# Performance work log

Hardware: AMD Instinct MI355X
Metric: run time of the kernel (lower is better)

Reference implementation:

```python
import jax, jax.numpy as jnp
import numpy as np

T, B, E, H, V = 128, 64, 300, 2048, 50000


def setup_inputs() -> dict:
    key = jax.random.key(0)
    ks = jax.random.split(key, 7)
    tokens = jax.random.randint(ks[0], (T, B), 0, V, dtype=jnp.int32)
    lens = jax.random.randint(ks[1], (B,), 1, T + 1, dtype=jnp.int32)  # lens >= 1 (assert 0 not in lens)
    embed_table = jax.random.normal(ks[2], (V, E), dtype=jnp.float32) * 0.1
    W_ih = jax.random.normal(ks[3], (4 * H, E), dtype=jnp.float32) * 0.02
    W_hh = jax.random.normal(ks[4], (4 * H, H), dtype=jnp.float32) * 0.02
    b_ih = jax.random.normal(ks[5], (4 * H,), dtype=jnp.float32) * 0.02
    b_hh = jax.random.normal(ks[6], (4 * H,), dtype=jnp.float32) * 0.02
    return {"tokens": tokens, "lens": lens, "embed_table": embed_table,
            "W_ih": W_ih, "W_hh": W_hh, "b_ih": b_ih, "b_hh": b_hh}


def _lstm_scan(xs, W_ih, W_hh, bias, reverse):
    # xs: [T, B, E]; returns all hidden states [T, B, H] (in scan order) and final (h, c)
    hdim = W_hh.shape[1]
    bsz = xs.shape[1]
    h0 = jnp.zeros((bsz, hdim), xs.dtype)
    c0 = jnp.zeros((bsz, hdim), xs.dtype)

    def step(carry, x):
        h, c = carry
        gates = x @ W_ih.T + h @ W_hh.T + bias  # [B, 4H]
        i, f, g, o = jnp.split(gates, 4, axis=-1)  # PyTorch LSTMCell gate order: i, f, g, o
        i = jax.nn.sigmoid(i)
        f = jax.nn.sigmoid(f)
        g = jnp.tanh(g)
        o = jax.nn.sigmoid(o)
        c = f * c + i * g
        h = o * jnp.tanh(c)
        return (h, c), h

    (h_fin, c_fin), hs = jax.lax.scan(step, (h0, c0), xs, reverse=reverse)
    return hs, h_fin


def reference(tokens, lens, embed_table, W_ih, W_hh, b_ih, b_hh):
    # tokens: [T, B] int ids (time-major, matching input_[i] loop over dim 0)
    x = embed_table[tokens]  # [T, B, E]
    bias = b_ih + b_hh
    hs_fwd, _ = _lstm_scan(x, W_ih, W_hh, bias, reverse=False)   # [T, B, H]
    _, h_bwd = _lstm_scan(x, W_ih, W_hh, bias, reverse=True)     # [B, H], same shared cell
    bsz = tokens.shape[1]
    # forward hidden at the last valid timestep of each example (lens - 1)
    last_fwd = hs_fwd[lens - 1, jnp.arange(bsz)]  # [B, H]
    return jnp.concatenate([last_fwd, h_bwd], axis=1)  # [B, 2H]
```

## Files before the change

### kernel.cpp

```cpp
#include <hip/hip_runtime.h>
#include <math.h>

#define T_ 128
#define B_ 64
#define E_ 300
#define H_ 2048

#define K1   2368
#define XKS  10
#define NKS  74
#define APELEMS 19398656ull
#define BXELEMS 5242880ull
#define BHPING  524288ull

typedef __attribute__((ext_vector_type(8))) short short8;
typedef __attribute__((ext_vector_type(4))) float float4v;

__device__ __forceinline__ unsigned f2bf(float f) {
    unsigned u = __float_as_uint(f);
    return (u + 0x7FFFu + ((u >> 16) & 1u)) >> 16;
}
__device__ __forceinline__ float bf2f(unsigned b) { return __uint_as_float(b << 16); }

__device__ __forceinline__ void gl_lds16(const void* g, void* l) {
    __builtin_amdgcn_global_load_lds(
        (const __attribute__((address_space(1))) unsigned int*)g,
        (__attribute__((address_space(3))) unsigned int*)l, 16, 0, 0);
}

__device__ __forceinline__ float sigm(float x) { return 1.f / (1.f + expf(-x)); }


__global__ void init2(short* __restrict__ Bh, float* __restrict__ cb) {
    const int nB = 2 * (int)BHPING;
    const int nC = 2 * 2048 * 64;
    int stride = gridDim.x * blockDim.x;
    int i = blockIdx.x * blockDim.x + threadIdx.x;
    for (int idx = i; idx < nB; idx += stride) Bh[idx] = 0;
    for (int idx = i; idx < nC; idx += stride) cb[idx] = 0.f;
}

__global__ void pack_w(const float* __restrict__ Wih, const float* __restrict__ Whh,
                       short* __restrict__ Ahi, short* __restrict__ Alo) {
    long long idx = (long long)blockIdx.x * blockDim.x + threadIdx.x;
    if (idx >= (long long)APELEMS) return;
    int j  = (int)(idx & 7);
    int l  = (int)((idx >> 3) & 63);
    int mf = (int)((idx >> 9) & 7);
    int rest = (int)(idx >> 12);
    int ks = rest % 74;
    int rb = rest / 74;
    int row = rb * 128 + mf * 16 + (l & 15);
    int kr  = ks * 32 + (l >> 4) * 8 + j;
    float wv = 0.f;
    if (kr < 300)       wv = Wih[(size_t)row * 300 + kr];
    else if (kr >= 320) wv = Whh[(size_t)row * 2048 + (kr - 320)];
    unsigned hb = f2bf(wv);
    Ahi[idx] = (short)hb;
    Alo[idx] = (short)f2bf(wv - bf2f(hb));
}

__global__ void pack_x(const int* __restrict__ tokens, const float* __restrict__ embed,
                       short* __restrict__ Bx) {
    long long idx = (long long)blockIdx.x * blockDim.x + threadIdx.x;
    if (idx >= (long long)BXELEMS) return;
    int j   = (int)(idx & 7);
    int l   = (int)((idx >> 3) & 63);
    int nf4 = (int)((idx >> 9) & 3);
    int hl  = (int)((idx >> 11) & 1);
    int rest = (int)(idx >> 12);
    int ks = rest % 10;
    int tt = rest / 10;
    int b  = nf4 * 16 + (l & 15);
    int kr = ks * 32 + (l >> 4) * 8 + j;
    float v = 0.f;
    if (kr < 300) {
        int tok = tokens[tt * 64 + b];
        v = embed[(size_t)tok * 300 + kr];
    }
    unsigned hb = f2bf(v);
    Bx[idx] = hl ? (short)f2bf(v - bf2f(hb)) : (short)hb;
}

template<int HI>
__device__ __forceinline__ void pass10(
    const short* __restrict__ ApB,
    const short* __restrict__ Bx,
    const short* __restrict__ BhP,
    short* lds, float4v (&acc)[4][4],
    int ks0, int nks, int t, int tid, int wm, int wn, int l, int boff)
{
    auto stage = [&](int ks, int buf) {
        short* As = lds + buf * 12288;
        short* Bs = As + 4096;
        const short* aB = ApB + (size_t)ks * 4096;
        gl_lds16(aB + tid * 8, As + tid * 8);
        gl_lds16(aB + 2048 + tid * 8, As + 2048 + tid * 8);
        constexpr int NBL = HI ? 4 : 2;
#pragma unroll
        for (int q = 0; q < NBL; ++q) {
            constexpr_int:;
            const int dsel = HI ? (q >> 1) : q;
            const int hl   = HI ? (q & 1) : 0;
            const short* base;
            if (ks < XKS) {
                const int xt = dsel ? (127 - t) : t;
                base = Bx + (size_t)(((xt * 10 + ks) * 2 + hl) * 4) * 512;
            } else {
                base = BhP + (size_t)((ks - 10) * 16 + (dsel * 2 + hl) * 4) * 512;
            }
            gl_lds16(base + boff, Bs + q * 2048 + tid * 8);
        }
    };

    stage(ks0, 0);
    stage(ks0 + 1, 1);
    if constexpr (HI) { asm volatile("s_waitcnt vmcnt(6)" ::: "memory"); }
    else              { asm volatile("s_waitcnt vmcnt(4)" ::: "memory"); }
    __builtin_amdgcn_s_barrier();
    __builtin_amdgcn_sched_barrier(0);

    for (int it = 0; it < nks; ++it) {
        const int buf = it % 3;
        stage(ks0 + it + 2, (it + 2) % 3);

        short* As = lds + buf * 12288;
        short* Bs = As + 4096;
        short8 a[4];
#pragma unroll
        for (int i = 0; i < 4; ++i)
            a[i] = *(const short8*)(As + ((wm * 4 + i) * 64 + l) * 8);

        if constexpr (HI) {
            short8 bf[8];
#pragma unroll
            for (int j = 0; j < 8; ++j)
                bf[j] = *(const short8*)(Bs + ((wn * 8 + j) * 64 + l) * 8);
            __builtin_amdgcn_s_setprio(1);
#pragma unroll
            for (int i = 0; i < 4; ++i)
#pragma unroll
                for (int h2 = 0; h2 < 2; ++h2)
#pragma unroll
                    for (int n = 0; n < 4; ++n)
                        acc[i][n] = __builtin_amdgcn_mfma_f32_16x16x32_bf16(
                            a[i], bf[h2 * 4 + n], acc[i][n], 0, 0, 0);
            __builtin_amdgcn_s_setprio(0);
        } else {
            short8 bf[4];
#pragma unroll
            for (int n = 0; n < 4; ++n)
                bf[n] = *(const short8*)(Bs + ((wn * 4 + n) * 64 + l) * 8);
            __builtin_amdgcn_s_setprio(1);
#pragma unroll
            for (int i = 0; i < 4; ++i)
#pragma unroll
                for (int n = 0; n < 4; ++n)
                    acc[i][n] = __builtin_amdgcn_mfma_f32_16x16x32_bf16(
                        a[i], bf[n], acc[i][n], 0, 0, 0);
            __builtin_amdgcn_s_setprio(0);
        }

        if constexpr (HI) { asm volatile("s_waitcnt vmcnt(6)" ::: "memory"); }
        else              { asm volatile("s_waitcnt vmcnt(4)" ::: "memory"); }
        __builtin_amdgcn_s_barrier();
        __builtin_amdgcn_sched_barrier(0);
    }

    asm volatile("s_waitcnt vmcnt(0)" ::: "memory");
    __builtin_amdgcn_s_barrier();
    __builtin_amdgcn_sched_barrier(0);
}

__global__ __launch_bounds__(256, 2) void gemm_step(
    const short* __restrict__ Ahi, const short* __restrict__ Alo,
    const short* __restrict__ Bx, const short* __restrict__ Bh,
    float* __restrict__ p, int t)
{
    __shared__ short lds[36864];
    const int bb = (int)blockIdx.x;
    const int mb = bb >> 3, s = bb & 7;
    const int tid = (int)threadIdx.x;
    const int w = tid >> 6, l = tid & 63;
    const int wm = w >> 1, wn = w & 1;
    const int ping = t & 1;
    const int ks0 = (s < 2) ? s * 10 : 20 + (s - 2) * 9;
    const int nks = (s < 2) ? 10 : 9;
    const int boff = w * 512 + l * 8;
    const short* BhP = Bh + (size_t)ping * BHPING;

    float4v acc[4][4];
#pragma unroll
    for (int i = 0; i < 4; ++i)
#pragma unroll
        for (int n = 0; n < 4; ++n) acc[i][n] = (float4v){0.f, 0.f, 0.f, 0.f};

    pass10<1>(Ahi + (size_t)mb * 74 * 4096, Bx, BhP, lds, acc,
              ks0, nks, t, tid, wm, wn, l, boff);
    pass10<0>(Alo + (size_t)mb * 74 * 4096, Bx, BhP, lds, acc,
              ks0, nks, t, tid, wm, wn, l, boff);

#pragma unroll
    for (int i = 0; i < 4; ++i)
#pragma unroll
        for (int n = 0; n < 4; ++n)
#pragma unroll
            for (int r = 0; r < 4; ++r) {
                int row = mb * 128 + wm * 64 + i * 16 + (l >> 4) * 4 + r;
                int col = wn * 64 + n * 16 + (l & 15);
                p[((size_t)s * 8192 + row) * 128 + col] = acc[i][n][r];
            }
}

__global__ __launch_bounds__(256) void update2(
    const float* __restrict__ p,
    const float* __restrict__ b_ih, const float* __restrict__ b_hh,
    const int* __restrict__ lens,
    float* __restrict__ cbuf,
    short* __restrict__ Bh,
    float* __restrict__ out, int t)
{
    int tid0 = blockIdx.x * 256 + threadIdx.x;
    for (int item = tid0; item < 262144; item += 65536) {
        int b = item & 63, k = (item >> 6) & 2047, dir = item >> 17;
        float g[4];
#pragma unroll
        for (int gg = 0; gg < 4; ++gg) {
            int row = gg * 2048 + k;
            float v = 0.f;
#pragma unroll
            for (int s = 0; s < 8; ++s) v += p[((size_t)s * 8192 + row) * 128 + dir * 64 + b];
            g[gg] = v + b_ih[row] + b_hh[row];
        }
        float iv = sigm(g[0]);
        float fv = sigm(g[1]);
        float gv = tanhf(g[2]);
        float ov = sigm(g[3]);
        size_t cidx = ((size_t)dir * 2048 + k) * 64 + b;
        float c = fv * cbuf[cidx] + iv * gv;
        cbuf[cidx] = c;
        float h = ov * tanhf(c);

        int kk = k & 31, ksh = k >> 5;
        int jj = kk & 7, ll = (kk >> 3) * 16 + (b & 15), sub = b >> 4;
        int pingW = (t + 1) & 1;
        size_t baseh = (size_t)pingW * BHPING + ((size_t)ksh * 16 + (dir * 2) * 4 + sub) * 512 + ll * 8 + jj;
        size_t basel = (size_t)pingW * BHPING + ((size_t)ksh * 16 + (dir * 2 + 1) * 4 + sub) * 512 + ll * 8 + jj;
        unsigned hb = f2bf(h);
        Bh[baseh] = (short)hb;
        Bh[basel] = (short)f2bf(h - bf2f(hb));

        if (dir == 0) { if (t == lens[b] - 1) out[(size_t)b * 4096 + k] = h; }
        else          { if (t == 127)         out[(size_t)b * 4096 + 2048 + k] = h; }
    }
}

#define R2K1    2368
#define R2EPAD  304
#define R2HOFF  304
#define R2HEND  2352
#define R2SEGSTEPS 74
#define R2REALSTEPS 222
#define R2SPLITSTEPS 56

__global__ void init_ws2(short* __restrict__ hb, float* __restrict__ cb,
                         short* __restrict__ zer) {
    const int nH = 2 * 2 * 2 * 64 * 2048;
    const int nC = 2 * 2048 * 64;
    int stride = gridDim.x * blockDim.x;
    int i = blockIdx.x * blockDim.x + threadIdx.x;
    for (int idx = i; idx < nH; idx += stride) hb[idx] = 0;
    for (int idx = i; idx < nC; idx += stride) cb[idx] = 0.f;
    for (int idx = i; idx < 128; idx += stride) zer[idx] = 0;
}

__global__ void conv_w(const float* __restrict__ Wih, const float* __restrict__ Whh,
                       short* __restrict__ whi, short* __restrict__ wlo) {
    int idx = blockIdx.x * blockDim.x + threadIdx.x;
    const int total = 8192 * R2K1;
    if (idx >= total) return;
    int j = idx / R2K1;
    int col = idx - j * R2K1;
    float w = 0.f;
    if (col < E_) w = Wih[(size_t)j * E_ + col];
    else if (col >= R2HOFF && col < R2HEND) w = Whh[(size_t)j * H_ + (col - R2HOFF)];
    unsigned hb = f2bf(w);
    whi[idx] = (short)hb;
    wlo[idx] = (short)f2bf(w - bf2f(hb));
}

__global__ void conv_x(const int* __restrict__ tokens, const float* __restrict__ embed,
                       short* __restrict__ xhi, short* __restrict__ xlo) {
    int idx = blockIdx.x * blockDim.x + threadIdx.x;
    const int total = T_ * B_ * R2EPAD;
    if (idx >= total) return;
    int t = idx / (B_ * R2EPAD);
    int r = idx - t * (B_ * R2EPAD);
    int bb = r / R2EPAD;
    int e = r - bb * R2EPAD;
    float v = 0.f;
    if (e < E_) {
        int tok = tokens[t * B_ + bb];
        v = embed[(size_t)tok * E_ + e];
    }
    unsigned hb = f2bf(v);
    xhi[idx] = (short)hb;
    xlo[idx] = (short)f2bf(v - bf2f(hb));
}

__global__ __launch_bounds__(512) void gemm_partial(
    const short* __restrict__ Whi, const short* __restrict__ Wlo,
    const short* __restrict__ xhi, const short* __restrict__ xlo,
    const short* __restrict__ hbuf,
    const short* __restrict__ zeros,
    float* __restrict__ pbuf, int t)
{
    __shared__ short As[2][8192];
    __shared__ short Bs[2][2048];

    const int bx  = blockIdx.x;
    const int s   = bx & 3;
    const int kt  = (bx >> 2) & 31;
    const int dir = bx >> 7;
    const int tid = threadIdx.x;
    const int w   = tid >> 6;
    const int l   = tid & 63;
    const int ping = t & 1;
    const int xt   = dir ? (T_ - 1 - t) : t;

    int jA[2], cA[2];
#pragma unroll
    for (int q = 0; q < 2; ++q) {
        int idx = (w * 2 + q) * 64 + l;
        cA[q] = idx >> 8;
        int row = idx & 255;
        jA[q] = (row >> 6) * 2048 + kt * 64 + (row & 63);
    }
    int cB = 0, bB = 0;
    if (w < 4) { int idx = w * 64 + l; cB = idx >> 6; bB = idx & 63; }

    const int lhi = l >> 4, llo = l & 15;
    const int rowbase = (w >> 1) * 64 + (w & 1) * 32;

    float4v acc[2][4];
#pragma unroll
    for (int a = 0; a < 2; ++a)
#pragma unroll
        for (int b = 0; b < 4; ++b) acc[a][b] = (float4v){0.f, 0.f, 0.f, 0.f};

    auto stage = [&](int g, int buf) {
        const bool dummy = (g >= R2REALSTEPS);
        const int seg = dummy ? 2 : g / R2SEGSTEPS;
        const int ss  = dummy ? 0 : g - seg * R2SEGSTEPS;
        const int kbase = ss * 32;
        const short* Wsel = (seg < 2) ? Whi : Wlo;
        const int hl = (seg == 1) ? 1 : 0;
        const short* xsel = (seg == 1) ? xlo : xhi;
        const short* hsel = hbuf + (((size_t)ping * 2 + hl) * 2 + dir) * (64 * 2048);
#pragma unroll
        for (int q = 0; q < 2; ++q) {
            const short* src = Wsel + (size_t)jA[q] * R2K1 + kbase + 8 * cA[q];
            gl_lds16(src, &As[buf][(w * 2 + q) * 64 * 8]);
        }
        if (w < 4) {
            int row8 = kbase + 8 * cB;
            const short* src;
            if (dummy || row8 >= R2HEND) src = zeros;
            else if (row8 < R2EPAD)      src = xsel + ((size_t)xt * 64 + bB) * R2EPAD + row8;
            else                         src = hsel + (size_t)bB * 2048 + (row8 - R2HOFF);
            gl_lds16(src, &Bs[buf][w * 64 * 8]);
        }
    };

    const int g0 = s * R2SPLITSTEPS;
    stage(g0, 0);

    for (int it = 0; it < R2SPLITSTEPS; ++it) {
        const int buf = it & 1;
        if (it + 1 < R2SPLITSTEPS) stage(g0 + it + 1, buf ^ 1);
        __syncthreads();
        short8 a0 = *(const short8*)&As[buf][(lhi * 256 + rowbase + llo) * 8];
        short8 a1 = *(const short8*)&As[buf][(lhi * 256 + rowbase + 16 + llo) * 8];
        short8 b0 = *(const short8*)&Bs[buf][(lhi * 64 + llo) * 8];
        short8 b1 = *(const short8*)&Bs[buf][(lhi * 64 + 16 + llo) * 8];
        short8 b2 = *(const short8*)&Bs[buf][(lhi * 64 + 32 + llo) * 8];
        short8 b3 = *(const short8*)&Bs[buf][(lhi * 64 + 48 + llo) * 8];
        acc[0][0] = __builtin_amdgcn_mfma_f32_16x16x32_bf16(a0, b0, acc[0][0], 0, 0, 0);
        acc[0][1] = __builtin_amdgcn_mfma_f32_16x16x32_bf16(a0, b1, acc[0][1], 0, 0, 0);
        acc[0][2] = __builtin_amdgcn_mfma_f32_16x16x32_bf16(a0, b2, acc[0][2], 0, 0, 0);
        acc[0][3] = __builtin_amdgcn_mfma_f32_16x16x32_bf16(a0, b3, acc[0][3], 0, 0, 0);
        acc[1][0] = __builtin_amdgcn_mfma_f32_16x16x32_bf16(a1, b0, acc[1][0], 0, 0, 0);
        acc[1][1] = __builtin_amdgcn_mfma_f32_16x16x32_bf16(a1, b1, acc[1][1], 0, 0, 0);
        acc[1][2] = __builtin_amdgcn_mfma_f32_16x16x32_bf16(a1, b2, acc[1][2], 0, 0, 0);
        acc[1][3] = __builtin_amdgcn_mfma_f32_16x16x32_bf16(a1, b3, acc[1][3], 0, 0, 0);
        __syncthreads();
    }

    float* pb = pbuf + (((size_t)(dir * 32 + kt) * 4 + s) * 256) * 64;
#pragma unroll
    for (int qm = 0; qm < 2; ++qm)
#pragma unroll
        for (int nb = 0; nb < 4; ++nb)
#pragma unroll
            for (int r = 0; r < 4; ++r) {
                int row = rowbase + qm * 16 + lhi * 4 + r;
                int col = nb * 16 + llo;
                pb[row * 64 + col] = acc[qm][nb][r];
            }
}

__global__ __launch_bounds__(256) void lstm_update(
    const float* __restrict__ pbuf,
    const float* __restrict__ b_ih, const float* __restrict__ b_hh,
    const int* __restrict__ lens,
    float* __restrict__ cbuf,
    short* __restrict__ hbuf,
    float* __restrict__ out, int t)
{
    const int bx = blockIdx.x;
    const int kt = bx & 31, dir = bx >> 5;
    const float* pb = pbuf + (size_t)(dir * 32 + kt) * 4 * 256 * 64;
    const int ping = (t + 1) & 1;

    for (int idx = threadIdx.x; idx < 4096; idx += 256) {
        const int q = idx >> 6, bb = idx & 63;
        const int k = kt * 64 + q;
        float gv[4];
#pragma unroll
        for (int gg = 0; gg < 4; ++gg) {
            const int r = gg * 64 + q;
            float v = 0.f;
#pragma unroll
            for (int s2 = 0; s2 < 4; ++s2) v += pb[(s2 * 256 + r) * 64 + bb];
            const int j = gg * 2048 + k;
            gv[gg] = v + b_ih[j] + b_hh[j];
        }
        const float iv = sigm(gv[0]);
        const float fv = sigm(gv[1]);
        const float g2 = tanhf(gv[2]);
        const float ov = sigm(gv[3]);
        const size_t cidx = ((size_t)dir * 2048 + k) * 64 + bb;
        const float c = fv * cbuf[cidx] + iv * g2;
        cbuf[cidx] = c;
        const float h = ov * tanhf(c);

        const unsigned hb = f2bf(h);
        const float hhi = bf2f(hb);
        const unsigned lb = f2bf(h - hhi);
        const size_t basehi = (((size_t)ping * 2 + 0) * 2 + dir) * (64 * 2048);
        const size_t baselo = (((size_t)ping * 2 + 1) * 2 + dir) * (64 * 2048);
        hbuf[basehi + (size_t)bb * 2048 + k] = (short)hb;
        hbuf[baselo + (size_t)bb * 2048 + k] = (short)lb;

        if (dir == 0) {
            if (t == lens[bb] - 1) out[(size_t)bb * (2 * H_) + k] = h;
        } else {
            if (t == T_ - 1) out[(size_t)bb * (2 * H_) + H_ + k] = h;
        }
    }
}

__global__ void init_state(float* __restrict__ hbuf, float* __restrict__ cbuf) {
    int n_h = 2 * 2 * H_ * B_;
    int n_c = 2 * H_ * B_;
    int stride = gridDim.x * blockDim.x;
    int i = blockIdx.x * blockDim.x + threadIdx.x;
    for (int idx = i; idx < n_h; idx += stride) hbuf[idx] = 0.f;
    for (int idx = i; idx < n_c; idx += stride) cbuf[idx] = 0.f;
}

__global__ void gather_x(const int* __restrict__ tokens, const float* __restrict__ embed,
                         float* __restrict__ x_t) {
    int idx = blockIdx.x * blockDim.x + threadIdx.x;
    int total = T_ * E_ * B_;
    if (idx >= total) return;
    int b = idx % B_;
    int r = idx / B_;
    int e = r % E_;
    int t = r / E_;
    int tok = tokens[t * B_ + b];
    x_t[idx] = embed[tok * E_ + e];
}

__global__ __launch_bounds__(256) void lstm_step(
    const float* __restrict__ x_t, const float* __restrict__ W_ih,
    const float* __restrict__ W_hh, const float* __restrict__ b_ih,
    const float* __restrict__ b_hh, const int* __restrict__ lens,
    const float* __restrict__ h_in, float* __restrict__ h_out,
    float* __restrict__ cbuf, float* __restrict__ out, int t)
{
    const int dir = blockIdx.x >> 8;
    const int kblk = blockIdx.x & 255;
    const int bpair = threadIdx.x & 31;
    const int kloc = threadIdx.x >> 5;
    const int k = kblk * 8 + kloc;
    const int b0 = bpair * 2;
    const int xt = dir ? (T_ - 1 - t) : t;
    const float* xrow = x_t + (size_t)xt * E_ * B_;
    const float* hrow = h_in + (size_t)dir * H_ * B_;
    float a0x = 0.f, a0y = 0.f, a1x = 0.f, a1y = 0.f;
    float a2x = 0.f, a2y = 0.f, a3x = 0.f, a3y = 0.f;
    {
        const float* w0 = W_ih + (size_t)(0 * H_ + k) * E_;
        const float* w1 = W_ih + (size_t)(1 * H_ + k) * E_;
        const float* w2 = W_ih + (size_t)(2 * H_ + k) * E_;
        const float* w3 = W_ih + (size_t)(3 * H_ + k) * E_;
#pragma unroll 4
        for (int kk = 0; kk < E_; ++kk) {
            float2 xv = *(const float2*)(xrow + kk * B_ + b0);
            float c0 = w0[kk], c1 = w1[kk], c2 = w2[kk], c3 = w3[kk];
            a0x += xv.x * c0; a0y += xv.y * c0;
            a1x += xv.x * c1; a1y += xv.y * c1;
            a2x += xv.x * c2; a2y += xv.y * c2;
            a3x += xv.x * c3; a3y += xv.y * c3;
        }
    }
    {
        const float* w0 = W_hh + (size_t)(0 * H_ + k) * H_;
        const float* w1 = W_hh + (size_t)(1 * H_ + k) * H_;
        const float* w2 = W_hh + (size_t)(2 * H_ + k) * H_;
        const float* w3 = W_hh + (size_t)(3 * H_ + k) * H_;
#pragma unroll 4
        for (int kk = 0; kk < H_; ++kk) {
            float2 hv = *(const float2*)(hrow + kk * B_ + b0);
            float c0 = w0[kk], c1 = w1[kk], c2 = w2[kk], c3 = w3[kk];
            a0x += hv.x * c0; a0y += hv.y * c0;
            a1x += hv.x * c1; a1y += hv.y * c1;
            a2x += hv.x * c2; a2y += hv.y * c2;
            a3x += hv.x * c3; a3y += hv.y * c3;
        }
    }
    const int j0 = 0 * H_ + k, j1 = 1 * H_ + k, j2 = 2 * H_ + k, j3 = 3 * H_ + k;
    const float bi = b_ih[j0] + b_hh[j0];
    const float bf = b_ih[j1] + b_hh[j1];
    const float bg = b_ih[j2] + b_hh[j2];
    const float bo = b_ih[j3] + b_hh[j3];
    float* cdir = cbuf + (size_t)dir * H_ * B_;
    float* hdir = h_out + (size_t)dir * H_ * B_;
#pragma unroll
    for (int s = 0; s < 2; ++s) {
        const int b = b0 + s;
        const float ai = (s == 0) ? a0x : a0y;
        const float af = (s == 0) ? a1x : a1y;
        const float ag = (s == 0) ? a2x : a2y;
        const float ao = (s == 0) ? a3x : a3y;
        const float iv = sigm(ai + bi);
        const float fv = sigm(af + bf);
        const float gv = tanhf(ag + bg);
        const float ov = sigm(ao + bo);
        const int sidx = k * B_ + b;
        const float c_old = cdir[sidx];
        const float c_new = fv * c_old + iv * gv;
        cdir[sidx] = c_new;
        const float h_new = ov * tanhf(c_new);
        hdir[sidx] = h_new;
        if (dir == 0) {
            if (t == lens[b] - 1) out[(size_t)b * (2 * H_) + k] = h_new;
        } else {
            if (t == T_ - 1) out[(size_t)b * (2 * H_) + H_ + k] = h_new;
        }
    }
}

extern "C" void kernel_launch(void* const* d_in, const int* in_sizes, int n_in,
                              void* d_out, int out_size, void* d_ws, size_t ws_size,
                              hipStream_t stream) {
    const int*   tokens = (const int*)d_in[0];
    const int*   lens   = (const int*)d_in[1];
    const float* embed  = (const float*)d_in[2];
    const float* W_ih   = (const float*)d_in[3];
    const float* W_hh   = (const float*)d_in[4];
    const float* b_ih   = (const float*)d_in[5];
    const float* b_hh   = (const float*)d_in[6];
    float* out = (float*)d_out;

    short* Ahi = (short*)d_ws;
    short* Alo = Ahi + APELEMS;
    short* BxP = Alo + APELEMS;
    short* BhP = BxP + BXELEMS;
    float* cb2n = (float*)(BhP + 2 * BHPING);
    float* pP   = cb2n + 262144;
    const size_t req_new = (size_t)((char*)(pP + 8388608) - (char*)d_ws);

    const size_t SZ_W  = (size_t)8192 * R2K1;
    const size_t SZ_X  = (size_t)T_ * B_ * R2EPAD;
    const size_t SZ_HB = (size_t)2 * 2 * 2 * 64 * 2048;
    const size_t SZ_CB = (size_t)2 * 2048 * 64;
    const size_t SZ_PB = (size_t)64 * 4 * 256 * 64;
    short* Whi2  = (short*)d_ws;
    short* Wlo2  = Whi2 + SZ_W;
    short* xhiB = Wlo2 + SZ_W;
    short* xloB = xhiB + SZ_X;
    short* hb2  = xloB + SZ_X;
    short* zer  = hb2 + SZ_HB;
    float* cb2  = (float*)(zer + 128);
    float* pbuf = cb2 + SZ_CB;
    const size_t req_r2 = (size_t)((char*)(pbuf + SZ_PB) - (char*)d_ws);

    if (ws_size >= req_new) {
        init2<<<512, 256, 0, stream>>>(BhP, cb2n);
        pack_w<<<(int)((APELEMS + 255) / 256), 256, 0, stream>>>(W_ih, W_hh, Ahi, Alo);
        pack_x<<<(int)((BXELEMS + 255) / 256), 256, 0, stream>>>(tokens, embed, BxP);
        for (int t = 0; t < T_; ++t) {
            gemm_step<<<512, 256, 0, stream>>>(Ahi, Alo, BxP, BhP, pP, t);
            update2<<<256, 256, 0, stream>>>(pP, b_ih, b_hh, lens, cb2n, BhP, out, t);
        }
    } else if (ws_size >= req_r2) {
        init_ws2<<<1024, 256, 0, stream>>>(hb2, cb2, zer);
        {
            int total = 8192 * R2K1;
            conv_w<<<(total + 255) / 256, 256, 0, stream>>>(W_ih, W_hh, Whi2, Wlo2);
        }
        {
            int total = T_ * B_ * R2EPAD;
            conv_x<<<(total + 255) / 256, 256, 0, stream>>>(tokens, embed, xhiB, xloB);
        }
        for (int t = 0; t < T_; ++t) {
            gemm_partial<<<256, 512, 0, stream>>>(Whi2, Wlo2, xhiB, xloB, hb2, zer, pbuf, t);
            lstm_update<<<64, 256, 0, stream>>>(pbuf, b_ih, b_hh, lens, cb2, hb2, out, t);
        }
    } else {
        float* ws   = (float*)d_ws;
        float* x_t  = ws;
        float* hbuf = x_t + (size_t)T_ * E_ * B_;
        float* cbuf = hbuf + (size_t)2 * 2 * H_ * B_;
        init_state<<<256, 256, 0, stream>>>(hbuf, cbuf);
        {
            int total = T_ * E_ * B_;
            gather_x<<<(total + 255) / 256, 256, 0, stream>>>(tokens, embed, x_t);
        }
        for (int t = 0; t < T_; ++t) {
            const float* h_in  = hbuf + (size_t)(t & 1) * 2 * H_ * B_;
            float*       h_out = hbuf + (size_t)((t + 1) & 1) * 2 * H_ * B_;
            lstm_step<<<512, 256, 0, stream>>>(x_t, W_ih, W_hh, b_ih, b_hh, lens,
                                               h_in, h_out, cbuf, out, t);
        }
    }
}
```

Baseline: 4.005 ms.

## Vectorize LSTM update h writes per k-octet and stagger hi/lo GEMM passes

The update kernel now has each thread handle 8 consecutive hidden units for one batch element. It writes the bf16 hi/lo h values as single 16-byte short8 stores instead of scattered 2-byte stores, and reads lens once. The grid shrinks to 256 blocks of 128 threads, which lowers thread-level parallelism. Separately, the GEMM step alternates the order of its Ahi and Alo passes across blocks so neighbouring blocks do not stream the same weight half at the same moment.

```diff
diff --git a/kernel.cpp b/kernel.cpp
--- a/kernel.cpp
+++ b/kernel.cpp
@@ -99,7 +99,6 @@
         constexpr int NBL = HI ? 4 : 2;
 #pragma unroll
         for (int q = 0; q < NBL; ++q) {
-            constexpr_int:;
             const int dsel = HI ? (q >> 1) : q;
             const int hl   = HI ? (q & 1) : 0;
             const short* base;
@@ -195,10 +194,18 @@
 #pragma unroll
         for (int n = 0; n < 4; ++n) acc[i][n] = (float4v){0.f, 0.f, 0.f, 0.f};
 
-    pass10<1>(Ahi + (size_t)mb * 74 * 4096, Bx, BhP, lds, acc,
-              ks0, nks, t, tid, wm, wn, l, boff);
-    pass10<0>(Alo + (size_t)mb * 74 * 4096, Bx, BhP, lds, acc,
-              ks0, nks, t, tid, wm, wn, l, boff);
+    const int stag = (bb & 1) ^ ((bb >> 8) & 1);
+    if (stag == 0) {
+        pass10<1>(Ahi + (size_t)mb * 74 * 4096, Bx, BhP, lds, acc,
+                  ks0, nks, t, tid, wm, wn, l, boff);
+        pass10<0>(Alo + (size_t)mb * 74 * 4096, Bx, BhP, lds, acc,
+                  ks0, nks, t, tid, wm, wn, l, boff);
+    } else {
+        pass10<0>(Alo + (size_t)mb * 74 * 4096, Bx, BhP, lds, acc,
+                  ks0, nks, t, tid, wm, wn, l, boff);
+        pass10<1>(Ahi + (size_t)mb * 74 * 4096, Bx, BhP, lds, acc,
+                  ks0, nks, t, tid, wm, wn, l, boff);
+    }
 
 #pragma unroll
     for (int i = 0; i < 4; ++i)
@@ -212,7 +219,7 @@
             }
 }
 
-__global__ __launch_bounds__(256) void update2(
+__global__ __launch_bounds__(128) void update3(
     const float* __restrict__ p,
     const float* __restrict__ b_ih, const float* __restrict__ b_hh,
     const int* __restrict__ lens,
@@ -220,38 +227,75 @@
     short* __restrict__ Bh,
     float* __restrict__ out, int t)
 {
-    int tid0 = blockIdx.x * 256 + threadIdx.x;
-    for (int item = tid0; item < 262144; item += 65536) {
-        int b = item & 63, k = (item >> 6) & 2047, dir = item >> 17;
-        float g[4];
+    const int tid = (int)(blockIdx.x * 128 + threadIdx.x);
+    const int b    = tid & 63;
+    const int kOct = (tid >> 6) & 255;
+    const int dir  = tid >> 14;
+    const int k0   = kOct * 8;
+
+    float g[4][8];
+#pragma unroll
+    for (int gg = 0; gg < 4; ++gg)
+#pragma unroll
+        for (int j = 0; j < 8; ++j) g[gg][j] = 0.f;
+
+    for (int s = 0; s < 8; ++s) {
 #pragma unroll
         for (int gg = 0; gg < 4; ++gg) {
-            int row = gg * 2048 + k;
-            float v = 0.f;
-#pragma unroll
-            for (int s = 0; s < 8; ++s) v += p[((size_t)s * 8192 + row) * 128 + dir * 64 + b];
-            g[gg] = v + b_ih[row] + b_hh[row];
-        }
-        float iv = sigm(g[0]);
-        float fv = sigm(g[1]);
-        float gv = tanhf(g[2]);
-        float ov = sigm(g[3]);
-        size_t cidx = ((size_t)dir * 2048 + k) * 64 + b;
-        float c = fv * cbuf[cidx] + iv * gv;
+            const float* pr = p + ((size_t)s * 8192 + gg * 2048 + k0) * 128 + dir * 64 + b;
+#pragma unroll
+            for (int j = 0; j < 8; ++j)
+                g[gg][j] += pr[(size_t)j * 128];
+        }
+    }
+#pragma unroll
+    for (int gg = 0; gg < 4; ++gg)
+#pragma unroll
+        for (int j = 0; j < 8; ++j) {
+            int row = gg * 2048 + k0 + j;
+            g[gg][j] += b_ih[row] + b_hh[row];
+        }
+
+    const int ksh = k0 >> 5;
+    const int kk8 = (k0 & 31) >> 3;
+    const int ll  = kk8 * 16 + (b & 15);
+    const int sub = b >> 4;
+    const int pingW = (t + 1) & 1;
+    const int len_b = lens[b];
+
+    short8 vh, vl;
+    float outv[8];
+#pragma unroll
+    for (int j = 0; j < 8; ++j) {
+        const int k = k0 + j;
+        const float iv = sigm(g[0][j]);
+        const float fv = sigm(g[1][j]);
+        const float gv = tanhf(g[2][j]);
+        const float ov = sigm(g[3][j]);
+        const size_t cidx = ((size_t)dir * 2048 + k) * 64 + b;
+        const float c = fv * cbuf[cidx] + iv * gv;
         cbuf[cidx] = c;
-        float h = ov * tanhf(c);
-
-        int kk = k & 31, ksh = k >> 5;
-        int jj = kk & 7, ll = (kk >> 3) * 16 + (b & 15), sub = b >> 4;
-        int pingW = (t + 1) & 1;
-        size_t baseh = (size_t)pingW * BHPING + ((size_t)ksh * 16 + (dir * 2) * 4 + sub) * 512 + ll * 8 + jj;
-        size_t basel = (size_t)pingW * BHPING + ((size_t)ksh * 16 + (dir * 2 + 1) * 4 + sub) * 512 + ll * 8 + jj;
-        unsigned hb = f2bf(h);
-        Bh[baseh] = (short)hb;
-        Bh[basel] = (short)f2bf(h - bf2f(hb));
-
-        if (dir == 0) { if (t == lens[b] - 1) out[(size_t)b * 4096 + k] = h; }
-        else          { if (t == 127)         out[(size_t)b * 4096 + 2048 + k] = h; }
+        const float h = ov * tanhf(c);
+        const unsigned hb = f2bf(h);
+        vh[j] = (short)hb;
+        vl[j] = (short)f2bf(h - bf2f(hb));
+        outv[j] = h;
+    }
+    const size_t baseh = (size_t)pingW * BHPING + ((size_t)ksh * 16 + (dir * 2) * 4 + sub) * 512 + ll * 8;
+    const size_t basel = (size_t)pingW * BHPING + ((size_t)ksh * 16 + (dir * 2 + 1) * 4 + sub) * 512 + ll * 8;
+    *(short8*)(Bh + baseh) = vh;
+    *(short8*)(Bh + basel) = vl;
+
+    if (dir == 0) {
+        if (t == len_b - 1) {
+#pragma unroll
+            for (int j = 0; j < 8; ++j) out[(size_t)b * 4096 + k0 + j] = outv[j];
+        }
+    } else {
+        if (t == 127) {
+#pragma unroll
+            for (int j = 0; j < 8; ++j) out[(size_t)b * 4096 + 2048 + k0 + j] = outv[j];
+        }
     }
 }
 
@@ -603,7 +647,7 @@
         pack_x<<<(int)((BXELEMS + 255) / 256), 256, 0, stream>>>(tokens, embed, BxP);
         for (int t = 0; t < T_; ++t) {
             gemm_step<<<512, 256, 0, stream>>>(Ahi, Alo, BxP, BhP, pP, t);
-            update2<<<256, 256, 0, stream>>>(pP, b_ih, b_hh, lens, cb2n, BhP, out, t);
+            update3<<<256, 128, 0, stream>>>(pP, b_ih, b_hh, lens, cb2n, BhP, out, t);
         }
     } else if (ws_size >= req_r2) {
         init_ws2<<<1024, 256, 0, stream>>>(hb2, cb2, zer);
```

Result: slower. 4.241 ms (+5.9%).

## Fuse hi and lo weight passes into one double-buffered K loop

Applied to the files above, without the earlier changes.

The two separate passes over the K range (hi-part weights, then lo-part weights), each reloading the B tiles, are merged into one loop. Each stage now loads both the Ahi and Alo tiles plus all B tiles, so B is fetched from global memory once per k-slice instead of twice. Pipelining drops from triple to double buffering with a barrier before compute, which reduces prefetch depth and may expose more load latency.

```diff
diff --git a/kernel.cpp b/kernel.cpp
--- a/kernel.cpp
+++ b/kernel.cpp
@@ -82,102 +82,12 @@
     Bx[idx] = hl ? (short)f2bf(v - bf2f(hb)) : (short)hb;
 }
 
-template<int HI>
-__device__ __forceinline__ void pass10(
-    const short* __restrict__ ApB,
-    const short* __restrict__ Bx,
-    const short* __restrict__ BhP,
-    short* lds, float4v (&acc)[4][4],
-    int ks0, int nks, int t, int tid, int wm, int wn, int l, int boff)
-{
-    auto stage = [&](int ks, int buf) {
-        short* As = lds + buf * 12288;
-        short* Bs = As + 4096;
-        const short* aB = ApB + (size_t)ks * 4096;
-        gl_lds16(aB + tid * 8, As + tid * 8);
-        gl_lds16(aB + 2048 + tid * 8, As + 2048 + tid * 8);
-        constexpr int NBL = HI ? 4 : 2;
-#pragma unroll
-        for (int q = 0; q < NBL; ++q) {
-            constexpr_int:;
-            const int dsel = HI ? (q >> 1) : q;
-            const int hl   = HI ? (q & 1) : 0;
-            const short* base;
-            if (ks < XKS) {
-                const int xt = dsel ? (127 - t) : t;
-                base = Bx + (size_t)(((xt * 10 + ks) * 2 + hl) * 4) * 512;
-            } else {
-                base = BhP + (size_t)((ks - 10) * 16 + (dsel * 2 + hl) * 4) * 512;
-            }
-            gl_lds16(base + boff, Bs + q * 2048 + tid * 8);
-        }
-    };
-
-    stage(ks0, 0);
-    stage(ks0 + 1, 1);
-    if constexpr (HI) { asm volatile("s_waitcnt vmcnt(6)" ::: "memory"); }
-    else              { asm volatile("s_waitcnt vmcnt(4)" ::: "memory"); }
-    __builtin_amdgcn_s_barrier();
-    __builtin_amdgcn_sched_barrier(0);
-
-    for (int it = 0; it < nks; ++it) {
-        const int buf = it % 3;
-        stage(ks0 + it + 2, (it + 2) % 3);
-
-        short* As = lds + buf * 12288;
-        short* Bs = As + 4096;
-        short8 a[4];
-#pragma unroll
-        for (int i = 0; i < 4; ++i)
-            a[i] = *(const short8*)(As + ((wm * 4 + i) * 64 + l) * 8);
-
-        if constexpr (HI) {
-            short8 bf[8];
-#pragma unroll
-            for (int j = 0; j < 8; ++j)
-                bf[j] = *(const short8*)(Bs + ((wn * 8 + j) * 64 + l) * 8);
-            __builtin_amdgcn_s_setprio(1);
-#pragma unroll
-            for (int i = 0; i < 4; ++i)
-#pragma unroll
-                for (int h2 = 0; h2 < 2; ++h2)
-#pragma unroll
-                    for (int n = 0; n < 4; ++n)
-                        acc[i][n] = __builtin_amdgcn_mfma_f32_16x16x32_bf16(
-                            a[i], bf[h2 * 4 + n], acc[i][n], 0, 0, 0);
-            __builtin_amdgcn_s_setprio(0);
-        } else {
-            short8 bf[4];
-#pragma unroll
-            for (int n = 0; n < 4; ++n)
-                bf[n] = *(const short8*)(Bs + ((wn * 4 + n) * 64 + l) * 8);
-            __builtin_amdgcn_s_setprio(1);
-#pragma unroll
-            for (int i = 0; i < 4; ++i)
-#pragma unroll
-                for (int n = 0; n < 4; ++n)
-                    acc[i][n] = __builtin_amdgcn_mfma_f32_16x16x32_bf16(
-                        a[i], bf[n], acc[i][n], 0, 0, 0);
-            __builtin_amdgcn_s_setprio(0);
-        }
-
-        if constexpr (HI) { asm volatile("s_waitcnt vmcnt(6)" ::: "memory"); }
-        else              { asm volatile("s_waitcnt vmcnt(4)" ::: "memory"); }
-        __builtin_amdgcn_s_barrier();
-        __builtin_amdgcn_sched_barrier(0);
-    }
-
-    asm volatile("s_waitcnt vmcnt(0)" ::: "memory");
-    __builtin_amdgcn_s_barrier();
-    __builtin_amdgcn_sched_barrier(0);
-}
-
 __global__ __launch_bounds__(256, 2) void gemm_step(
     const short* __restrict__ Ahi, const short* __restrict__ Alo,
     const short* __restrict__ Bx, const short* __restrict__ Bh,
     float* __restrict__ p, int t)
 {
-    __shared__ short lds[36864];
+    __shared__ short lds[32768];
     const int bb = (int)blockIdx.x;
     const int mb = bb >> 3, s = bb & 7;
     const int tid = (int)threadIdx.x;
@@ -186,8 +96,9 @@
     const int ping = t & 1;
     const int ks0 = (s < 2) ? s * 10 : 20 + (s - 2) * 9;
     const int nks = (s < 2) ? 10 : 9;
-    const int boff = w * 512 + l * 8;
-    const short* BhP = Bh + (size_t)ping * BHPING;
+    const short* AhiB = Ahi + (size_t)mb * 74 * 4096;
+    const short* AloB = Alo + (size_t)mb * 74 * 4096;
+    const short* BhP  = Bh + (size_t)ping * BHPING;
 
     float4v acc[4][4];
 #pragma unroll
@@ -195,10 +106,73 @@
 #pragma unroll
         for (int n = 0; n < 4; ++n) acc[i][n] = (float4v){0.f, 0.f, 0.f, 0.f};
 
-    pass10<1>(Ahi + (size_t)mb * 74 * 4096, Bx, BhP, lds, acc,
-              ks0, nks, t, tid, wm, wn, l, boff);
-    pass10<0>(Alo + (size_t)mb * 74 * 4096, Bx, BhP, lds, acc,
-              ks0, nks, t, tid, wm, wn, l, boff);
+    auto stage = [&](int ks, int buf) {
+        short* As = lds + buf * 16384;
+        short* Al = As + 4096;
+        short* Bs = As + 8192;
+        const short* aH = AhiB + (size_t)ks * 4096;
+        const short* aL = AloB + (size_t)ks * 4096;
+        gl_lds16(aH + tid * 8,        As + tid * 8);
+        gl_lds16(aH + 2048 + tid * 8, As + 2048 + tid * 8);
+        gl_lds16(aL + tid * 8,        Al + tid * 8);
+        gl_lds16(aL + 2048 + tid * 8, Al + 2048 + tid * 8);
+#pragma unroll
+        for (int q = 0; q < 4; ++q) {
+            const int dsel = q >> 1, hl = q & 1;
+            const short* base;
+            if (ks < XKS) {
+                const int xt = dsel ? (127 - t) : t;
+                base = Bx + (size_t)(((xt * 10 + ks) * 2 + hl) * 4) * 512;
+            } else {
+                base = BhP + (size_t)((ks - 10) * 16 + (dsel * 2 + hl) * 4) * 512;
+            }
+            gl_lds16(base + tid * 8, Bs + q * 2048 + tid * 8);
+        }
+    };
+
+    stage(ks0, 0);
+    for (int it = 0; it < nks; ++it) {
+        stage(ks0 + it + 1, (it + 1) & 1);
+        asm volatile("s_waitcnt vmcnt(8)" ::: "memory");
+        __builtin_amdgcn_s_barrier();
+        __builtin_amdgcn_sched_barrier(0);
+
+        short* As = lds + (it & 1) * 16384;
+        short* Al = As + 4096;
+        short* Bs = As + 8192;
+        short8 ah[4], al[4], bf[8];
+#pragma unroll
+        for (int i = 0; i < 4; ++i) {
+            ah[i] = *(const short8*)(As + ((wm * 4 + i) * 64 + l) * 8);
+            al[i] = *(const short8*)(Al + ((wm * 4 + i) * 64 + l) * 8);
+        }
+#pragma unroll
+        for (int j = 0; j < 8; ++j)
+            bf[j] = *(const short8*)(Bs + ((wn * 8 + j) * 64 + l) * 8);
+
+        __builtin_amdgcn_s_setprio(1);
+#pragma unroll
+        for (int i = 0; i < 4; ++i)
+#pragma unroll
+            for (int h2 = 0; h2 < 2; ++h2)
+#pragma unroll
+                for (int n = 0; n < 4; ++n)
+                    acc[i][n] = __builtin_amdgcn_mfma_f32_16x16x32_bf16(
+                        ah[i], bf[h2 * 4 + n], acc[i][n], 0, 0, 0);
+#pragma unroll
+        for (int i = 0; i < 4; ++i)
+#pragma unroll
+            for (int n = 0; n < 4; ++n)
+                acc[i][n] = __builtin_amdgcn_mfma_f32_16x16x32_bf16(
+                    al[i], bf[n], acc[i][n], 0, 0, 0);
+        __builtin_amdgcn_s_setprio(0);
+
+        __builtin_amdgcn_s_barrier();
+        __builtin_amdgcn_sched_barrier(0);
+    }
+    asm volatile("s_waitcnt vmcnt(0)" ::: "memory");
+    __builtin_amdgcn_s_barrier();
+    __builtin_amdgcn_sched_barrier(0);
 
 #pragma unroll
     for (int i = 0; i < 4; ++i)
```

New measurement: 3.728 ms. 1.07x faster.
